# Optimization experiments

Hardware: AMD Instinct MI355X
Metric: run time of the kernel (lower is better)

The kernel has to match this reference:

```python
import jax, jax.numpy as jnp
import numpy as np

N = 8192
BOX = 50.0
CUTOFF = 5.0
MAX_E = 64 * N  # padded edge capacity (~34 avg neighbors expected)


def setup_inputs() -> dict:
    key = jax.random.key(0)
    pos = jax.random.uniform(key, (N, 3), dtype=jnp.float32) * BOX
    return {"pos": pos}


def _pairwise_dist(pos):
    # Euclidean cdist via the gram-matrix identity; avoids the [N,N,3] intermediate.
    sq = jnp.sum(pos * pos, axis=-1)                      # [N]
    d2 = sq[:, None] + sq[None, :] - 2.0 * (pos @ pos.T)  # [N,N]
    return jnp.sqrt(jnp.maximum(d2, 0.0))


def reference(pos):
    n = pos.shape[0]
    dist = _pairwise_dist(pos)
    # mask self-edges by pushing the diagonal above the cutoff (as in the torch code)
    dist = dist + (CUTOFF + 1.0) * jnp.eye(n, dtype=dist.dtype)
    mask = dist < CUTOFF
    # data-dependent nonzero -> fixed-size padded output for jit compatibility;
    # padded entries are filled with -1.
    rows, cols = jnp.nonzero(mask, size=MAX_E, fill_value=-1)
    return jnp.stack([rows, cols], axis=0)  # [2, MAX_E], int32
```

## Files before the change

kernel.cpp:

```cpp
#include <hip/hip_runtime.h>
#include <stdint.h>

#define N 8192
#define MAX_E (64 * N)
#define NCHUNK (N / 64)
#define TILE 2048
#define CTILES (N / TILE)
#define CPAIRS (TILE / 128)
#define ROWS_PER_WAVE 8
#define WAVES 4
#define ROWS_PER_BLOCK (ROWS_PER_WAVE * WAVES)
#define RGROUPS (N / ROWS_PER_BLOCK)
#define E_BLOCKS 512
#define E_ROWS 16

__device__ __forceinline__ float sq_exact(float x, float y, float z) {
    return __fadd_rn(__fadd_rn(__fmul_rn(x, x), __fmul_rn(y, y)), __fmul_rn(z, z));
}

__device__ __forceinline__ bool edge_pred(float xi, float yi, float zi, float sqi,
                                          const float4& pj) {
    float dot = __fmaf_rn(zi, pj.z, __fmaf_rn(yi, pj.y, __fmul_rn(xi, pj.x)));
    float d2  = __fmaf_rn(-2.0f, dot, __fadd_rn(sqi, pj.w));
    return d2 < 0x1.8ffffep+4f;
}

__global__ __launch_bounds__(256) void mask_kernel(const float* __restrict__ posf,
                                                   uint64_t* __restrict__ masks,
                                                   int* __restrict__ counts4) {
    __shared__ float4 pts[TILE];
    const int tid  = threadIdx.x;
    const int wave = tid >> 6;
    const int lane = tid & 63;
    const int row0 = blockIdx.x * ROWS_PER_BLOCK + wave * ROWS_PER_WAVE;
    const int ct   = blockIdx.y;
    const int cb   = ct * TILE;

    float xi[ROWS_PER_WAVE], yi[ROWS_PER_WAVE], zi[ROWS_PER_WAVE], sqi[ROWS_PER_WAVE];
    uint64_t k0[ROWS_PER_WAVE], k1[ROWS_PER_WAVE];
#pragma unroll
    for (int r = 0; r < ROWS_PER_WAVE; r++) {
        int i = row0 + r;
        xi[r] = posf[3 * i + 0];
        yi[r] = posf[3 * i + 1];
        zi[r] = posf[3 * i + 2];
        sqi[r] = sq_exact(xi[r], yi[r], zi[r]);
        k0[r] = 0; k1[r] = 0;
    }

    for (int k = tid; k < TILE; k += 256) {
        float x = posf[3 * (cb + k) + 0];
        float y = posf[3 * (cb + k) + 1];
        float z = posf[3 * (cb + k) + 2];
        pts[k] = make_float4(x, y, z, sq_exact(x, y, z));
    }
    __syncthreads();

    float4 pa = pts[lane];
    float4 pb = pts[64 + lane];
#pragma unroll 4
    for (int c = 0; c < TILE; c += 128) {
        float4 na = pts[((c + 128) & (TILE - 1)) + lane];
        float4 nb = pts[((c + 192) & (TILE - 1)) + lane];
        const int owner = c >> 7;
#pragma unroll
        for (int r = 0; r < ROWS_PER_WAVE; r++) {
            uint64_t ma = __ballot(edge_pred(xi[r], yi[r], zi[r], sqi[r], pa));
            if (lane == owner) k0[r] = ma;
            uint64_t mb = __ballot(edge_pred(xi[r], yi[r], zi[r], sqi[r], pb));
            if (lane == owner) k1[r] = mb;
        }
        pa = na; pb = nb;
    }

#pragma unroll
    for (int r = 0; r < ROWS_PER_WAVE; r++) {
        const int row = row0 + r;
        if ((row >> 11) == ct) {
            const int ls = (row & (TILE - 1)) >> 6;
            if (lane == (ls >> 1)) {
                uint64_t clr = ~(1ull << (row & 63));
                if (ls & 1) k1[r] &= clr; else k0[r] &= clr;
            }
        }
        if (lane < CPAIRS) {
            ulonglong2 v; v.x = k0[r]; v.y = k1[r];
            ((ulonglong2*)(masks + (size_t)row * NCHUNK))[ct * CPAIRS + lane] = v;
        }
        int t = __popcll(k0[r]) + __popcll(k1[r]);
#pragma unroll
        for (int o = 32; o > 0; o >>= 1) t += __shfl_down(t, o);
        if (lane == 0) counts4[row * CTILES + ct] = t;
    }
}

__global__ __launch_bounds__(256) void emit_kernel(const uint64_t* __restrict__ masks,
                                                   const int* __restrict__ counts4,
                                                   int* __restrict__ out) {
    const int tid  = threadIdx.x;
    const int wave = tid >> 6;
    const int lane = tid & 63;
    const int row0 = blockIdx.x * E_ROWS;

    __shared__ int part[256];
    __shared__ int roff[E_ROWS];
    __shared__ int Etot_s;

    const int4* c4 = (const int4*)counts4;
    int s = 0;
#pragma unroll 8
    for (int k = 0; k < 32; k++) {
        int4 v = c4[tid * 32 + k];
        s += v.x + v.y + v.z + v.w;
    }
    part[tid] = s;
    __syncthreads();
    for (int off = 1; off < 256; off <<= 1) {
        int v = (tid >= off) ? part[tid - off] : 0;
        __syncthreads();
        part[tid] += v;
        __syncthreads();
    }
    if (tid < E_ROWS) {
        const int ch = row0 >> 5;
        int off = (ch > 0) ? part[ch - 1] : 0;
        for (int rr = (ch << 5); rr < row0 + tid; rr++) {
            int4 v = c4[rr];
            off += v.x + v.y + v.z + v.w;
        }
        roff[tid] = off;
    }
    if (tid == 0) Etot_s = part[255];
    __syncthreads();

    const int E = Etot_s;
    for (int idx = E + blockIdx.x * 256 + tid; idx < MAX_E; idx += E_BLOCKS * 256) {
        out[idx] = -1; out[MAX_E + idx] = -1;
    }

#pragma unroll
    for (int r = 0; r < 4; r++) {
        const int lr  = wave * 4 + r;
        const int row = row0 + lr;
        ulonglong2 v = ((const ulonglong2*)(masks + (size_t)row * NCHUNK))[lane];
        int s0 = __popcll(v.x), s1 = __popcll(v.y);
        int x = s0 + s1;
#pragma unroll
        for (int o = 1; o < 64; o <<= 1) {
            int t = __shfl_up(x, o);
            if (lane >= o) x += t;
        }
        int slot = roff[lr] + (x - (s0 + s1));

        const int col0 = lane * 128;
        uint64_t m = v.x;
        while (m) {
            int b = __ffsll((unsigned long long)m) - 1;
            m &= m - 1;
            if (slot < MAX_E) { out[slot] = row; out[MAX_E + slot] = col0 + b; }
            slot++;
        }
        m = v.y;
        while (m) {
            int b = __ffsll((unsigned long long)m) - 1;
            m &= m - 1;
            if (slot < MAX_E) { out[slot] = row; out[MAX_E + slot] = col0 + 64 + b; }
            slot++;
        }
    }
}

extern "C" void kernel_launch(void* const* d_in, const int* in_sizes, int n_in,
                              void* d_out, int out_size, void* d_ws, size_t ws_size,
                              hipStream_t stream) {
    const float* posf = (const float*)d_in[0];
    int* out = (int*)d_out;
    int* counts4 = (int*)d_ws;
    uint64_t* masks = (uint64_t*)((char*)d_ws + (512 << 10));

    dim3 grid(RGROUPS, CTILES);
    mask_kernel<<<grid, 256, 0, stream>>>(posf, masks, counts4);
    emit_kernel<<<E_BLOCKS, 256, 0, stream>>>(masks, counts4, out);
}
```

Before: 91.19 us.

## Replace all-pairs mask computation with uniform cell-list neighbor search

Adds a single-block binning kernel that assigns points to a 9x9x9 grid of cells at least as wide as the cutoff and counting-sorts them by cell. The mask kernel then tests each row only against points in the 27 neighboring cells, setting bits in a shared bitmask through LDS atomics instead of running the dense N^2 predicate with ballots. This removes most of the quadratic distance work. In exchange it adds a serial single-block binning stage, atomics and irregular gathers.

```diff
diff --git a/kernel.cpp b/kernel.cpp
--- a/kernel.cpp
+++ b/kernel.cpp
@@ -4,13 +4,10 @@
 #define N 8192
 #define MAX_E (64 * N)
 #define NCHUNK (N / 64)
-#define TILE 2048
-#define CTILES (N / TILE)
-#define CPAIRS (TILE / 128)
-#define ROWS_PER_WAVE 8
-#define WAVES 4
-#define ROWS_PER_BLOCK (ROWS_PER_WAVE * WAVES)
-#define RGROUPS (N / ROWS_PER_BLOCK)
+#define NCELL1 9
+#define NCELLS (NCELL1 * NCELL1 * NCELL1)
+#define SCALE (9.0f / 50.0f)
+#define M_WAVES 4
 #define E_BLOCKS 512
 #define E_ROWS 16
 
@@ -25,77 +22,103 @@
     return d2 < 0x1.8ffffep+4f;
 }
 
+__device__ __forceinline__ int cell_of(float v) {
+    int c = (int)(__fmul_rn(v, SCALE));
+    return c > 8 ? 8 : c;
+}
+
+__global__ __launch_bounds__(1024) void bin_kernel(const float* __restrict__ posf,
+                                                   int* __restrict__ cellid,
+                                                   int* __restrict__ cell_start,
+                                                   float4* __restrict__ sortedf4,
+                                                   int* __restrict__ sortedIdx) {
+    __shared__ int hist[NCELLS];
+    __shared__ int sc[1024];
+    const int tid = threadIdx.x;
+    for (int c = tid; c < NCELLS; c += 1024) hist[c] = 0;
+    __syncthreads();
+    for (int i = tid; i < N; i += 1024) {
+        float x = posf[3 * i], y = posf[3 * i + 1], z = posf[3 * i + 2];
+        int c = (cell_of(x) * NCELL1 + cell_of(y)) * NCELL1 + cell_of(z);
+        cellid[i] = c;
+        atomicAdd(&hist[c], 1);
+    }
+    __syncthreads();
+    sc[tid] = (tid < NCELLS) ? hist[tid] : 0;
+    __syncthreads();
+    for (int off = 1; off < 1024; off <<= 1) {
+        int v = (tid >= off) ? sc[tid - off] : 0;
+        __syncthreads();
+        sc[tid] += v;
+        __syncthreads();
+    }
+    int excl = (tid > 0) ? sc[tid - 1] : 0;
+    __syncthreads();
+    if (tid < NCELLS) { hist[tid] = excl; cell_start[tid] = excl; }
+    if (tid == NCELLS) cell_start[NCELLS] = sc[NCELLS - 1];
+    __syncthreads();
+    for (int i = tid; i < N; i += 1024) {
+        float x = posf[3 * i], y = posf[3 * i + 1], z = posf[3 * i + 2];
+        int p = atomicAdd(&hist[cellid[i]], 1);
+        sortedf4[p] = make_float4(x, y, z, sq_exact(x, y, z));
+        sortedIdx[p] = i;
+    }
+}
+
 __global__ __launch_bounds__(256) void mask_kernel(const float* __restrict__ posf,
+                                                   const int* __restrict__ cell_start,
+                                                   const float4* __restrict__ sortedf4,
+                                                   const int* __restrict__ sortedIdx,
                                                    uint64_t* __restrict__ masks,
-                                                   int* __restrict__ counts4) {
-    __shared__ float4 pts[TILE];
+                                                   int* __restrict__ counts) {
+    __shared__ uint32_t lmask[M_WAVES][256];
     const int tid  = threadIdx.x;
     const int wave = tid >> 6;
     const int lane = tid & 63;
-    const int row0 = blockIdx.x * ROWS_PER_BLOCK + wave * ROWS_PER_WAVE;
-    const int ct   = blockIdx.y;
-    const int cb   = ct * TILE;
-
-    float xi[ROWS_PER_WAVE], yi[ROWS_PER_WAVE], zi[ROWS_PER_WAVE], sqi[ROWS_PER_WAVE];
-    uint64_t k0[ROWS_PER_WAVE], k1[ROWS_PER_WAVE];
-#pragma unroll
-    for (int r = 0; r < ROWS_PER_WAVE; r++) {
-        int i = row0 + r;
-        xi[r] = posf[3 * i + 0];
-        yi[r] = posf[3 * i + 1];
-        zi[r] = posf[3 * i + 2];
-        sqi[r] = sq_exact(xi[r], yi[r], zi[r]);
-        k0[r] = 0; k1[r] = 0;
-    }
-
-    for (int k = tid; k < TILE; k += 256) {
-        float x = posf[3 * (cb + k) + 0];
-        float y = posf[3 * (cb + k) + 1];
-        float z = posf[3 * (cb + k) + 2];
-        pts[k] = make_float4(x, y, z, sq_exact(x, y, z));
-    }
-    __syncthreads();
-
-    float4 pa = pts[lane];
-    float4 pb = pts[64 + lane];
-#pragma unroll 4
-    for (int c = 0; c < TILE; c += 128) {
-        float4 na = pts[((c + 128) & (TILE - 1)) + lane];
-        float4 nb = pts[((c + 192) & (TILE - 1)) + lane];
-        const int owner = c >> 7;
-#pragma unroll
-        for (int r = 0; r < ROWS_PER_WAVE; r++) {
-            uint64_t ma = __ballot(edge_pred(xi[r], yi[r], zi[r], sqi[r], pa));
-            if (lane == owner) k0[r] = ma;
-            uint64_t mb = __ballot(edge_pred(xi[r], yi[r], zi[r], sqi[r], pb));
-            if (lane == owner) k1[r] = mb;
-        }
-        pa = na; pb = nb;
-    }
-
-#pragma unroll
-    for (int r = 0; r < ROWS_PER_WAVE; r++) {
-        const int row = row0 + r;
-        if ((row >> 11) == ct) {
-            const int ls = (row & (TILE - 1)) >> 6;
-            if (lane == (ls >> 1)) {
-                uint64_t clr = ~(1ull << (row & 63));
-                if (ls & 1) k1[r] &= clr; else k0[r] &= clr;
+    const int row  = blockIdx.x * M_WAVES + wave;
+
+#pragma unroll
+    for (int k = lane; k < 256; k += 64) lmask[wave][k] = 0;
+
+    const float xi = posf[3 * row], yi = posf[3 * row + 1], zi = posf[3 * row + 2];
+    const float sqi = sq_exact(xi, yi, zi);
+    const int cx = cell_of(xi), cy = cell_of(yi), cz = cell_of(zi);
+    const int z0 = (cz > 0) ? cz - 1 : 0;
+    const int zcnt = ((cz < 8) ? cz + 1 : 8) - z0 + 1;
+    __syncthreads();
+
+    for (int dxy = 0; dxy < 9; dxy++) {
+        const int nx = cx + dxy / 3 - 1;
+        const int ny = cy + dxy % 3 - 1;
+        if ((unsigned)nx > 8u || (unsigned)ny > 8u) continue;
+        const int c0  = (nx * NCELL1 + ny) * NCELL1 + z0;
+        const int beg = cell_start[c0];
+        const int end = cell_start[c0 + zcnt];
+        for (int base = beg; base < end; base += 64) {
+            const int k = base + lane;
+            if (k < end) {
+                float4 pj = sortedf4[k];
+                int j = sortedIdx[k];
+                if (j != row && edge_pred(xi, yi, zi, sqi, pj))
+                    atomicOr(&lmask[wave][j >> 5], 1u << (j & 31));
             }
         }
-        if (lane < CPAIRS) {
-            ulonglong2 v; v.x = k0[r]; v.y = k1[r];
-            ((ulonglong2*)(masks + (size_t)row * NCHUNK))[ct * CPAIRS + lane] = v;
-        }
-        int t = __popcll(k0[r]) + __popcll(k1[r]);
-#pragma unroll
-        for (int o = 32; o > 0; o >>= 1) t += __shfl_down(t, o);
-        if (lane == 0) counts4[row * CTILES + ct] = t;
-    }
+    }
+    __syncthreads();
+
+    uint4 u = ((const uint4*)lmask[wave])[lane];
+    uint64_t k0 = (uint64_t)u.x | ((uint64_t)u.y << 32);
+    uint64_t k1 = (uint64_t)u.z | ((uint64_t)u.w << 32);
+    ulonglong2 v; v.x = k0; v.y = k1;
+    ((ulonglong2*)(masks + (size_t)row * NCHUNK))[lane] = v;
+    int t = __popcll(k0) + __popcll(k1);
+#pragma unroll
+    for (int o = 32; o > 0; o >>= 1) t += __shfl_down(t, o);
+    if (lane == 0) counts[row] = t;
 }
 
 __global__ __launch_bounds__(256) void emit_kernel(const uint64_t* __restrict__ masks,
-                                                   const int* __restrict__ counts4,
+                                                   const int* __restrict__ counts,
                                                    int* __restrict__ out) {
     const int tid  = threadIdx.x;
     const int wave = tid >> 6;
@@ -106,11 +129,11 @@
     __shared__ int roff[E_ROWS];
     __shared__ int Etot_s;
 
-    const int4* c4 = (const int4*)counts4;
+    const int4* c4 = (const int4*)counts;
     int s = 0;
-#pragma unroll 8
-    for (int k = 0; k < 32; k++) {
-        int4 v = c4[tid * 32 + k];
+#pragma unroll
+    for (int k = 0; k < 8; k++) {
+        int4 v = c4[tid * 8 + k];
         s += v.x + v.y + v.z + v.w;
     }
     part[tid] = s;
@@ -124,10 +147,7 @@
     if (tid < E_ROWS) {
         const int ch = row0 >> 5;
         int off = (ch > 0) ? part[ch - 1] : 0;
-        for (int rr = (ch << 5); rr < row0 + tid; rr++) {
-            int4 v = c4[rr];
-            off += v.x + v.y + v.z + v.w;
-        }
+        for (int rr = (ch << 5); rr < row0 + tid; rr++) off += counts[rr];
         roff[tid] = off;
     }
     if (tid == 0) Etot_s = part[255];
@@ -175,10 +195,16 @@
                               hipStream_t stream) {
     const float* posf = (const float*)d_in[0];
     int* out = (int*)d_out;
-    int* counts4 = (int*)d_ws;
-    uint64_t* masks = (uint64_t*)((char*)d_ws + (512 << 10));
-
-    dim3 grid(RGROUPS, CTILES);
-    mask_kernel<<<grid, 256, 0, stream>>>(posf, masks, counts4);
-    emit_kernel<<<E_BLOCKS, 256, 0, stream>>>(masks, counts4, out);
-}
+    char* ws = (char*)d_ws;
+    int*      counts     = (int*)ws;
+    int*      cell_start = (int*)(ws + (64 << 10));
+    int*      cellid     = (int*)(ws + (128 << 10));
+    int*      sortedIdx  = (int*)(ws + (192 << 10));
+    float4*   sortedf4   = (float4*)(ws + (256 << 10));
+    uint64_t* masks      = (uint64_t*)(ws + (512 << 10));
+
+    bin_kernel<<<1, 1024, 0, stream>>>(posf, cellid, cell_start, sortedf4, sortedIdx);
+    mask_kernel<<<N / M_WAVES, 256, 0, stream>>>(posf, cell_start, sortedf4,
+                                                 sortedIdx, masks, counts);
+    emit_kernel<<<E_BLOCKS, 256, 0, stream>>>(masks, counts, out);
+}
```

Result: no change. 91.74 us (+0.6%).
